# Kernel optimization log

Measured on AMD Instinct MI355X. Metric: run time of the kernel, lower is better.

## Reference

```python
import jax, jax.numpy as jnp
import numpy as np

N, F, HID, H, B = 400000, 128, 32, 4, 2000

def setup_inputs() -> dict:
    key = jax.random.key(0)
    ks = jax.random.split(key, 8)
    atom_fea = jax.random.normal(ks[0], (N, F), dtype=jnp.float32)
    segment_ids = jnp.sort(jax.random.randint(ks[1], (N,), 0, B, dtype=jnp.int32))
    s = 0.05
    return {
        "atom_fea": atom_fea,
        "segment_ids": segment_ids,
        "num_crystals": B,
        "W1": jax.random.normal(ks[2], (F, HID), dtype=jnp.float32) * s,
        "b1": jnp.zeros((HID,), dtype=jnp.float32),
        "W2": jax.random.normal(ks[3], (HID, H), dtype=jnp.float32) * s,
        "b2": jnp.zeros((H,), dtype=jnp.float32),
        "Wp": jax.random.normal(ks[4], (H * F, F), dtype=jnp.float32) * s,
        "bp": jnp.zeros((F,), dtype=jnp.float32),
    }

def reference(atom_fea, segment_ids, num_crystals, W1, b1, W2, b2, Wp, bp):
    # key MLP: (N,F) -> (N,H) attention logits (dropout is eval no-op)
    logits = jax.nn.silu(atom_fea @ W1 + b1) @ W2 + b2  # (N,H)
    # segment softmax over atoms within each crystal, per head
    seg_max = jax.ops.segment_max(logits, segment_ids, num_segments=num_crystals)
    ex = jnp.exp(logits - seg_max[segment_ids])
    denom = jax.ops.segment_sum(ex, segment_ids, num_segments=num_crystals)
    w = ex / denom[segment_ids]  # (N,H)
    # per-head softmax-weighted segment sum of atom features -> (B,H,F)
    weighted = jax.ops.segment_sum(
        w[:, :, None] * atom_fea[:, None, :], segment_ids, num_segments=num_crystals
    )
    flat = weighted.reshape(num_crystals, -1)  # (B, H*F)
    return jax.nn.silu(flat @ Wp + bp)  # (B,F)
```

## Files before the change

### kernel.cpp

```cpp
#include <hip/hip_runtime.h>
#include <math.h>

#define F 128
#define HID 32
#define NH 4
#define TILE 32
#define ROWB 512
#define PJC 4

typedef __attribute__((ext_vector_type(8))) short bf16x8;
typedef __attribute__((ext_vector_type(4))) float f32x4;

__device__ __forceinline__ float silu_f(float x) {
    return x / (1.0f + __expf(-x));
}

__device__ __forceinline__ uint f2bf(float f) {
    union { float f; uint u; } v; v.f = f;
    uint r = v.u + 0x7fffu + ((v.u >> 16) & 1u);
    return r >> 16;
}

__device__ __forceinline__ uint cvtpk_bf16(float lo, float hi) {
    uint r;
    asm("v_cvt_pk_bf16_f32 %0, %1, %2" : "=v"(r) : "v"(lo), "v"(hi));
    return r;
}

__device__ __forceinline__ void gload_lds16(const void* g, void* l) {
    __builtin_amdgcn_global_load_lds(
        (const __attribute__((address_space(1))) void*)g,
        (__attribute__((address_space(3))) void*)l, 16, 0, 0);
}

__global__ void seg_starts_kernel(const int* __restrict__ seg, int* __restrict__ starts,
                                  int N, int B) {
    int i = blockIdx.x * blockDim.x + threadIdx.x;
    if (i >= N) return;
    int id = seg[i];
    if (i == 0) {
        for (int b = 0; b <= id; ++b) starts[b] = 0;
    } else {
        int prev = seg[i - 1];
        for (int b = prev + 1; b <= id; ++b) starts[b] = i;
    }
    if (i == N - 1) {
        for (int b = id + 1; b <= B; ++b) starts[b] = N;
    }
}

__global__ __launch_bounds__(256, 4) void fused9_kernel(
    const float* __restrict__ atom_fea, const int* __restrict__ starts,
    const float* __restrict__ W1, const float* __restrict__ b1,
    const float* __restrict__ W2, const float* __restrict__ b2,
    float* __restrict__ gWacc) {
    __shared__ float sStage[2][TILE * F];
    __shared__ float sP[2 * TILE * 5];
    __shared__ float sTW[NH * 65];

    const int t = threadIdx.x;
    const int b = blockIdx.x;
    const int start = starts[b];
    const int end = starts[b + 1];
    const int wv = t >> 6;
    const int lane = t & 63;
    const int lg = lane >> 4;
    const int l15 = lane & 15;
    const int ag = wv & 1;
    const int mh = wv >> 1;
    const int ca = lane & 3;
    const int co = (lane >> 2) & 15;

    int roff[4], coff[4];
    #pragma unroll
    for (int i = 0; i < 4; ++i) {
        const int q = i * 256 + t;
        roff[i] = q >> 5;
        coff[i] = ((q & 31) ^ (roff[i] & 7)) << 4;
    }

    bf16x8 w1f[4];
    #pragma unroll
    for (int kk = 0; kk < 4; ++kk) {
        bf16x8 fr;
        #pragma unroll
        for (int j = 0; j < 8; ++j)
            fr[j] = (short)f2bf(W1[(kk * 32 + lg * 8 + j) * HID + mh * 16 + l15]);
        w1f[kk] = fr;
    }
    float b1r[4], w2r[4][4];
    #pragma unroll
    for (int r = 0; r < 4; ++r) {
        const int h = mh * 16 + lg * 4 + r;
        b1r[r] = b1[h];
        #pragma unroll
        for (int j = 0; j < 4; ++j) w2r[r][j] = W2[h * NH + j];
    }
    const float b2w = b2[wv];

    float m_run = -INFINITY;
    float s_part = 0.0f;
    float acc8[8] = {0, 0, 0, 0, 0, 0, 0, 0};

    const int nt = (end > start) ? (end - start + TILE - 1) / TILE : 0;
    const char* gbase = (const char*)atom_fea;

    if (nt > 0) {
        #pragma unroll
        for (int i = 0; i < 4; ++i) {
            int a = start + roff[i]; a = (a < end) ? a : end - 1;
            gload_lds16(gbase + (size_t)a * ROWB + coff[i],
                        (char*)sStage[0] + i * 4096 + wv * 1024);
        }
    }
    __syncthreads();

    int pb = 0;
    for (int ti = 0; ti < nt; ++ti) {
        const int base = start + ti * TILE;
        const int T = min(TILE, end - base);
        const char* bufc = (const char*)sStage[pb];
        const bool has_next = (ti + 1 < nt);

        if (has_next) {
            const int nbase = base + TILE;
            char* ldst = (char*)sStage[pb ^ 1];
            #pragma unroll
            for (int i = 0; i < 4; ++i) {
                int a = nbase + roff[i]; a = (a < end) ? a : end - 1;
                gload_lds16(gbase + (size_t)a * ROWB + coff[i],
                            ldst + i * 4096 + wv * 1024);
            }
        }

        {
            f32x4 acc;
            #pragma unroll
            for (int r = 0; r < 4; ++r) acc[r] = b1r[r];
            const int row = ag * 16 + l15;
            const char* rb = bufc + row * ROWB;
            const int rs = row & 7;
            #pragma unroll
            for (int kk = 0; kk < 4; ++kk) {
                const int c0 = kk * 8 + lg * 2;
                const float4 va = *(const float4*)(rb + ((c0 ^ rs) << 4));
                const float4 vb = *(const float4*)(rb + (((c0 + 1) ^ rs) << 4));
                union { bf16x8 v; uint u[4]; } fr;
                fr.u[0] = cvtpk_bf16(va.x, va.y);
                fr.u[1] = cvtpk_bf16(va.z, va.w);
                fr.u[2] = cvtpk_bf16(vb.x, vb.y);
                fr.u[3] = cvtpk_bf16(vb.z, vb.w);
                acc = __builtin_amdgcn_mfma_f32_16x16x32_bf16(w1f[kk], fr.v, acc, 0, 0, 0);
            }
            float p0 = 0, p1 = 0, p2 = 0, p3 = 0;
            #pragma unroll
            for (int r = 0; r < 4; ++r) {
                const float s = silu_f(acc[r]);
                p0 = fmaf(s, w2r[r][0], p0);
                p1 = fmaf(s, w2r[r][1], p1);
                p2 = fmaf(s, w2r[r][2], p2);
                p3 = fmaf(s, w2r[r][3], p3);
            }
            p0 += __shfl_xor(p0, 16); p0 += __shfl_xor(p0, 32);
            p1 += __shfl_xor(p1, 16); p1 += __shfl_xor(p1, 32);
            p2 += __shfl_xor(p2, 16); p2 += __shfl_xor(p2, 32);
            p3 += __shfl_xor(p3, 16); p3 += __shfl_xor(p3, 32);
            if (lane < 16) {
                float* d = &sP[(mh * TILE + ag * 16 + lane) * 5];
                d[0] = p0; d[1] = p1; d[2] = p2; d[3] = p3;
            }
        }
        asm volatile("s_waitcnt lgkmcnt(0)" ::: "memory");
        __builtin_amdgcn_s_barrier();

        {
            const float v = (lane < T)
                ? sP[lane * 5 + wv] + sP[(TILE + lane) * 5 + wv] + b2w
                : -INFINITY;
            if (__any(v > m_run + 8.0f)) {
                float mt = v;
                #pragma unroll
                for (int d = 1; d < 64; d <<= 1) mt = fmaxf(mt, __shfl_xor(mt, d));
                const float m_new = fmaxf(m_run, mt);
                const float r = __expf(m_run - m_new);
                s_part *= r;
                #pragma unroll
                for (int j = 0; j < 8; ++j) acc8[j] *= r;
                m_run = m_new;
            }
            const float e = (lane < T) ? __expf(v - m_run) : 0.0f;
            sTW[wv * 65 + lane] = e;
            s_part += e;
        }

        {
            #pragma unroll 4
            for (int i = 0; i < 8; ++i) {
                const int a = i * 4 + ca;
                const float w = sTW[wv * 65 + a];
                const int sw = a & 7;
                const char* ra = bufc + a * ROWB;
                const float4 v0 = *(const float4*)(ra + (((2 * co) ^ sw) << 4));
                const float4 v1 = *(const float4*)(ra + (((2 * co + 1) ^ sw) << 4));
                acc8[0] = fmaf(w, v0.x, acc8[0]);
                acc8[1] = fmaf(w, v0.y, acc8[1]);
                acc8[2] = fmaf(w, v0.z, acc8[2]);
                acc8[3] = fmaf(w, v0.w, acc8[3]);
                acc8[4] = fmaf(w, v1.x, acc8[4]);
                acc8[5] = fmaf(w, v1.y, acc8[5]);
                acc8[6] = fmaf(w, v1.z, acc8[6]);
                acc8[7] = fmaf(w, v1.w, acc8[7]);
            }
        }
        __syncthreads();
        pb ^= 1;
    }

    #pragma unroll
    for (int d = 1; d < 64; d <<= 1) s_part += __shfl_xor(s_part, d);
    const float inv = (s_part > 0.0f) ? 1.0f / s_part : 0.0f;
    #pragma unroll
    for (int j = 0; j < 8; ++j) {
        acc8[j] += __shfl_xor(acc8[j], 1);
        acc8[j] += __shfl_xor(acc8[j], 2);
    }
    if ((lane & 3) == 0) {
        float* dst = &gWacc[(size_t)b * 512 + wv * F + (lane >> 2) * 8];
        *(float4*)dst = make_float4(acc8[0] * inv, acc8[1] * inv, acc8[2] * inv, acc8[3] * inv);
        *(float4*)(dst + 4) = make_float4(acc8[4] * inv, acc8[5] * inv, acc8[6] * inv, acc8[7] * inv);
    }
}

__global__ __launch_bounds__(256) void proj_kernel(
    const float* __restrict__ gWacc, const float* __restrict__ Wp,
    const float* __restrict__ bp, float* __restrict__ out, int B) {
    __shared__ float sW[PJC * 512];
    __shared__ float sP[256 * PJC];
    const int t = threadIdx.x;
    const int c0 = blockIdx.x * PJC;
    for (int q = t; q < PJC * 512; q += 256) {
        const int cr = c0 + (q >> 9);
        sW[q] = (cr < B) ? gWacc[(size_t)cr * 512 + (q & 511)] : 0.0f;
    }
    __syncthreads();
    const int f = t & 127, half = t >> 7;
    float acc[PJC] = {};
    const float* wp = Wp + (size_t)(half * 256) * F + f;
    for (int k0 = 0; k0 < 256; k0 += 8) {
        float wpv[8];
        #pragma unroll
        for (int u = 0; u < 8; ++u) wpv[u] = wp[(size_t)(k0 + u) * F];
        #pragma unroll
        for (int u = 0; u < 8; ++u) {
            const int ks = half * 256 + k0 + u;
            #pragma unroll
            for (int g = 0; g < PJC; ++g) acc[g] = fmaf(sW[g * 512 + ks], wpv[u], acc[g]);
        }
    }
    #pragma unroll
    for (int g = 0; g < PJC; ++g) sP[t * PJC + g] = acc[g];
    __syncthreads();
    if (t < 128) {
        const float bpf = bp[t];
        #pragma unroll
        for (int g = 0; g < PJC; ++g) {
            const int cr = c0 + g;
            if (cr < B)
                out[(size_t)cr * F + t] =
                    silu_f(sP[t * PJC + g] + sP[(t + 128) * PJC + g] + bpf);
        }
    }
}

extern "C" void kernel_launch(void* const* d_in, const int* in_sizes, int n_in,
                              void* d_out, int out_size, void* d_ws, size_t ws_size,
                              hipStream_t stream) {
    const float* atom_fea = (const float*)d_in[0];
    const int* seg = (const int*)d_in[1];
    const float* W1 = (const float*)d_in[3];
    const float* b1 = (const float*)d_in[4];
    const float* W2 = (const float*)d_in[5];
    const float* b2 = (const float*)d_in[6];
    const float* Wp = (const float*)d_in[7];
    const float* bp = (const float*)d_in[8];
    float* out = (float*)d_out;

    const int N = in_sizes[0] / F;
    const int B = out_size / F;

    char* ws = (char*)d_ws;
    int* starts = (int*)ws;
    size_t off = (((size_t)(B + 1) * sizeof(int)) + 255) & ~(size_t)255;
    float* gWacc = (float*)(ws + off);

    seg_starts_kernel<<<(N + 255) / 256, 256, 0, stream>>>(seg, starts, N, B);
    fused9_kernel<<<B, 256, 0, stream>>>(atom_fea, starts, W1, b1, W2, b2, gWacc);
    proj_kernel<<<(B + PJC - 1) / PJC, 256, 0, stream>>>(gWacc, Wp, bp, out, B);
}
```

Measured before the change: 64.72 us.

## Repartition weighted-sum work: waves split atoms, lanes cover heads and feature chunks

The weighted accumulation is remapped so each wave handles a slice of 8 atoms, and the four lane groups within a wave each take one head, instead of each wave owning one head and walking all atoms. This gives every wave distinct rows of the shared-memory tile, with the same 8 rows read for all four heads, so LDS reads of atom features are shared across heads. Softmax rescale factors and the final normalisers are now passed through shared memory. The price is an extra barrier per tile and a final cross-wave reduction through LDS.

```diff
diff --git a/kernel.cpp b/kernel.cpp
--- a/kernel.cpp
+++ b/kernel.cpp
@@ -49,7 +49,7 @@
     }
 }
 
-__global__ __launch_bounds__(256, 4) void fused9_kernel(
+__global__ __launch_bounds__(256, 4) void fused10_kernel(
     const float* __restrict__ atom_fea, const int* __restrict__ starts,
     const float* __restrict__ W1, const float* __restrict__ b1,
     const float* __restrict__ W2, const float* __restrict__ b2,
@@ -57,6 +57,8 @@
     __shared__ float sStage[2][TILE * F];
     __shared__ float sP[2 * TILE * 5];
     __shared__ float sTW[NH * 65];
+    __shared__ float sR[NH];
+    __shared__ float sInv[NH];
 
     const int t = threadIdx.x;
     const int b = blockIdx.x;
@@ -68,8 +70,8 @@
     const int l15 = lane & 15;
     const int ag = wv & 1;
     const int mh = wv >> 1;
-    const int ca = lane & 3;
-    const int co = (lane >> 2) & 15;
+    const int ch = lane & 3;
+    const int co = lane >> 2;
 
     int roff[4], coff[4];
     #pragma unroll
@@ -177,27 +179,33 @@
             const float v = (lane < T)
                 ? sP[lane * 5 + wv] + sP[(TILE + lane) * 5 + wv] + b2w
                 : -INFINITY;
+            float r_t = 1.0f;
             if (__any(v > m_run + 8.0f)) {
                 float mt = v;
                 #pragma unroll
                 for (int d = 1; d < 64; d <<= 1) mt = fmaxf(mt, __shfl_xor(mt, d));
                 const float m_new = fmaxf(m_run, mt);
-                const float r = __expf(m_run - m_new);
-                s_part *= r;
-                #pragma unroll
-                for (int j = 0; j < 8; ++j) acc8[j] *= r;
+                r_t = __expf(m_run - m_new);
+                s_part *= r_t;
                 m_run = m_new;
             }
+            if (lane == 0) sR[wv] = r_t;
             const float e = (lane < T) ? __expf(v - m_run) : 0.0f;
             sTW[wv * 65 + lane] = e;
             s_part += e;
         }
+        asm volatile("s_waitcnt lgkmcnt(0)" ::: "memory");
+        __builtin_amdgcn_s_barrier();
 
         {
+            const float rr = sR[ch];
+            #pragma unroll
+            for (int j = 0; j < 8; ++j) acc8[j] *= rr;
+            const int abase = wv * 8;
             #pragma unroll 4
             for (int i = 0; i < 8; ++i) {
-                const int a = i * 4 + ca;
-                const float w = sTW[wv * 65 + a];
+                const int a = abase + i;
+                const float w = sTW[ch * 65 + a];
                 const int sw = a & 7;
                 const char* ra = bufc + a * ROWB;
                 const float4 v0 = *(const float4*)(ra + (((2 * co) ^ sw) << 4));
@@ -218,16 +226,24 @@
 
     #pragma unroll
     for (int d = 1; d < 64; d <<= 1) s_part += __shfl_xor(s_part, d);
-    const float inv = (s_part > 0.0f) ? 1.0f / s_part : 0.0f;
-    #pragma unroll
-    for (int j = 0; j < 8; ++j) {
-        acc8[j] += __shfl_xor(acc8[j], 1);
-        acc8[j] += __shfl_xor(acc8[j], 2);
-    }
-    if ((lane & 3) == 0) {
-        float* dst = &gWacc[(size_t)b * 512 + wv * F + (lane >> 2) * 8];
-        *(float4*)dst = make_float4(acc8[0] * inv, acc8[1] * inv, acc8[2] * inv, acc8[3] * inv);
-        *(float4*)(dst + 4) = make_float4(acc8[4] * inv, acc8[5] * inv, acc8[6] * inv, acc8[7] * inv);
+    if (lane == 0) sInv[wv] = (s_part > 0.0f) ? 1.0f / s_part : 0.0f;
+
+    float* red = (float*)sStage[0];
+    *(float4*)&red[(wv * 64 + lane) * 8] = make_float4(acc8[0], acc8[1], acc8[2], acc8[3]);
+    *(float4*)&red[(wv * 64 + lane) * 8 + 4] = make_float4(acc8[4], acc8[5], acc8[6], acc8[7]);
+    __syncthreads();
+    if (t < 64) {
+        const int rh = t & 3, ro = t >> 2;
+        const float inv = sInv[rh];
+        float o[8];
+        #pragma unroll
+        for (int j = 0; j < 8; ++j) {
+            o[j] = (red[(0 * 64 + t) * 8 + j] + red[(1 * 64 + t) * 8 + j] +
+                    red[(2 * 64 + t) * 8 + j] + red[(3 * 64 + t) * 8 + j]) * inv;
+        }
+        float* dst = &gWacc[(size_t)b * 512 + rh * F + ro * 8];
+        *(float4*)dst = make_float4(o[0], o[1], o[2], o[3]);
+        *(float4*)(dst + 4) = make_float4(o[4], o[5], o[6], o[7]);
     }
 }
 
@@ -294,6 +310,6 @@
     float* gWacc = (float*)(ws + off);
 
     seg_starts_kernel<<<(N + 255) / 256, 256, 0, stream>>>(seg, starts, N, B);
-    fused9_kernel<<<B, 256, 0, stream>>>(atom_fea, starts, W1, b1, W2, b2, gWacc);
+    fused10_kernel<<<B, 256, 0, stream>>>(atom_fea, starts, W1, b1, W2, b2, gWacc);
     proj_kernel<<<(B + PJC - 1) / PJC, 256, 0, stream>>>(gWacc, Wp, bp, out, B);
 }
```

Result: no change. 65.49 us (+1.2%).

## Give each wave its own row slice and merge per-wave softmax states in an epilogue

Applied to the files above, without the earlier changes.

Each of the four waves now streams and processes its own 16-row slice of a 64-row block tile into a private double buffer. It computes all 32 hidden units and all 4 head logits itself and keeps per-wave online-softmax state for every head. This removes the block-wide barriers and the cross-wave logit exchange inside the tile loop. The per-wave maxima, sums and accumulators are then combined through shared memory in a final epilogue. The cost is doubled shared memory per block (launch bounds lowered to 2 blocks), twice the MFMA work per wave, and idle waves on short segment tails.

```diff
diff --git a/kernel.cpp b/kernel.cpp
--- a/kernel.cpp
+++ b/kernel.cpp
@@ -4,7 +4,8 @@
 #define F 128
 #define HID 32
 #define NH 4
-#define TILE 32
+#define WTILE 16
+#define BTILE 64
 #define ROWB 512
 #define PJC 4
 
@@ -49,14 +50,13 @@
     }
 }
 
-__global__ __launch_bounds__(256, 4) void fused9_kernel(
+__global__ __launch_bounds__(256, 2) void fused11_kernel(
     const float* __restrict__ atom_fea, const int* __restrict__ starts,
     const float* __restrict__ W1, const float* __restrict__ b1,
     const float* __restrict__ W2, const float* __restrict__ b2,
     float* __restrict__ gWacc) {
-    __shared__ float sStage[2][TILE * F];
-    __shared__ float sP[2 * TILE * 5];
-    __shared__ float sTW[NH * 65];
+    __shared__ float sBuf[NH][2][WTILE * F];
+    __shared__ float sTW[NH][WTILE * NH];
 
     const int t = threadIdx.x;
     const int b = blockIdx.x;
@@ -66,80 +66,77 @@
     const int lane = t & 63;
     const int lg = lane >> 4;
     const int l15 = lane & 15;
-    const int ag = wv & 1;
-    const int mh = wv >> 1;
-    const int ca = lane & 3;
-    const int co = (lane >> 2) & 15;
-
-    int roff[4], coff[4];
+    const int ch = lane & 3;
+    const int co = lane >> 2;
+    const int lrh = lane >> 5;
+    const int lch = lane & 31;
+
+    bf16x8 w1f[2][4];
     #pragma unroll
-    for (int i = 0; i < 4; ++i) {
-        const int q = i * 256 + t;
-        roff[i] = q >> 5;
-        coff[i] = ((q & 31) ^ (roff[i] & 7)) << 4;
-    }
-
-    bf16x8 w1f[4];
+    for (int m0 = 0; m0 < 2; ++m0)
+        #pragma unroll
+        for (int kk = 0; kk < 4; ++kk) {
+            bf16x8 fr;
+            #pragma unroll
+            for (int j = 0; j < 8; ++j)
+                fr[j] = (short)f2bf(W1[(kk * 32 + lg * 8 + j) * HID + m0 * 16 + l15]);
+            w1f[m0][kk] = fr;
+        }
+    float b1r[8], w2r[8][4];
     #pragma unroll
-    for (int kk = 0; kk < 4; ++kk) {
-        bf16x8 fr;
-        #pragma unroll
-        for (int j = 0; j < 8; ++j)
-            fr[j] = (short)f2bf(W1[(kk * 32 + lg * 8 + j) * HID + mh * 16 + l15]);
-        w1f[kk] = fr;
-    }
-    float b1r[4], w2r[4][4];
-    #pragma unroll
-    for (int r = 0; r < 4; ++r) {
-        const int h = mh * 16 + lg * 4 + r;
-        b1r[r] = b1[h];
-        #pragma unroll
-        for (int j = 0; j < 4; ++j) w2r[r][j] = W2[h * NH + j];
-    }
-    const float b2w = b2[wv];
-
-    float m_run = -INFINITY;
-    float s_part = 0.0f;
+    for (int m0 = 0; m0 < 2; ++m0)
+        #pragma unroll
+        for (int r = 0; r < 4; ++r) {
+            const int h = m0 * 16 + lg * 4 + r;
+            b1r[m0 * 4 + r] = b1[h];
+            #pragma unroll
+            for (int j = 0; j < 4; ++j) w2r[m0 * 4 + r][j] = W2[h * NH + j];
+        }
+    const float b2r0 = b2[0], b2r1 = b2[1], b2r2 = b2[2], b2r3 = b2[3];
+
+    float m0_ = -INFINITY, m1_ = -INFINITY, m2_ = -INFINITY, m3_ = -INFINITY;
+    float s0_ = 0.0f, s1_ = 0.0f, s2_ = 0.0f, s3_ = 0.0f;
     float acc8[8] = {0, 0, 0, 0, 0, 0, 0, 0};
 
-    const int nt = (end > start) ? (end - start + TILE - 1) / TILE : 0;
-    const char* gbase = (const char*)atom_fea;
+    const int nt = (end > start) ? (end - start + BTILE - 1) / BTILE : 0;
+    const char* gb = (const char*)atom_fea;
+    char* bufA = (char*)&sBuf[wv][0][0];
+    char* bufB = (char*)&sBuf[wv][1][0];
 
     if (nt > 0) {
         #pragma unroll
-        for (int i = 0; i < 4; ++i) {
-            int a = start + roff[i]; a = (a < end) ? a : end - 1;
-            gload_lds16(gbase + (size_t)a * ROWB + coff[i],
-                        (char*)sStage[0] + i * 4096 + wv * 1024);
-        }
-    }
-    __syncthreads();
+        for (int i = 0; i < 8; ++i) {
+            const int lr = 2 * i + lrh;
+            int ga = start + wv * WTILE + lr; ga = (ga < end) ? ga : end - 1;
+            gload_lds16(gb + (size_t)ga * ROWB + ((lch ^ (lr & 7)) << 4), bufA + i * 1024);
+        }
+    }
+    asm volatile("s_waitcnt vmcnt(0)" ::: "memory");
 
     int pb = 0;
     for (int ti = 0; ti < nt; ++ti) {
-        const int base = start + ti * TILE;
-        const int T = min(TILE, end - base);
-        const char* bufc = (const char*)sStage[pb];
-        const bool has_next = (ti + 1 < nt);
-
-        if (has_next) {
-            const int nbase = base + TILE;
-            char* ldst = (char*)sStage[pb ^ 1];
-            #pragma unroll
-            for (int i = 0; i < 4; ++i) {
-                int a = nbase + roff[i]; a = (a < end) ? a : end - 1;
-                gload_lds16(gbase + (size_t)a * ROWB + coff[i],
-                            ldst + i * 4096 + wv * 1024);
-            }
-        }
-
-        {
-            f32x4 acc;
-            #pragma unroll
-            for (int r = 0; r < 4; ++r) acc[r] = b1r[r];
-            const int row = ag * 16 + l15;
-            const char* rb = bufc + row * ROWB;
-            const int rs = row & 7;
+        const int base = start + ti * BTILE;
+        const int T = min(BTILE, end - base);
+        const int Tw = min(T - wv * WTILE, WTILE);
+        char* bufc = pb ? bufB : bufA;
+
+        if (ti + 1 < nt) {
+            char* bufn = pb ? bufA : bufB;
+            const int nb = base + BTILE;
+            #pragma unroll
+            for (int i = 0; i < 8; ++i) {
+                const int lr = 2 * i + lrh;
+                int ga = nb + wv * WTILE + lr; ga = (ga < end) ? ga : end - 1;
+                gload_lds16(gb + (size_t)ga * ROWB + ((lch ^ (lr & 7)) << 4), bufn + i * 1024);
+            }
+        }
+
+        if (Tw > 0) {
+            f32x4 a0, a1;
+            #pragma unroll
+            for (int r = 0; r < 4; ++r) { a0[r] = b1r[r]; a1[r] = b1r[4 + r]; }
+            const char* rb = bufc + l15 * ROWB;
+            const int rs = l15 & 7;
             #pragma unroll
             for (int kk = 0; kk < 4; ++kk) {
                 const int c0 = kk * 8 + lg * 2;
@@ -150,84 +147,118 @@
                 fr.u[1] = cvtpk_bf16(va.z, va.w);
                 fr.u[2] = cvtpk_bf16(vb.x, vb.y);
                 fr.u[3] = cvtpk_bf16(vb.z, vb.w);
-                acc = __builtin_amdgcn_mfma_f32_16x16x32_bf16(w1f[kk], fr.v, acc, 0, 0, 0);
+                a0 = __builtin_amdgcn_mfma_f32_16x16x32_bf16(w1f[0][kk], fr.v, a0, 0, 0, 0);
+                a1 = __builtin_amdgcn_mfma_f32_16x16x32_bf16(w1f[1][kk], fr.v, a1, 0, 0, 0);
             }
             float p0 = 0, p1 = 0, p2 = 0, p3 = 0;
             #pragma unroll
             for (int r = 0; r < 4; ++r) {
-                const float s = silu_f(acc[r]);
-                p0 = fmaf(s, w2r[r][0], p0);
-                p1 = fmaf(s, w2r[r][1], p1);
-                p2 = fmaf(s, w2r[r][2], p2);
-                p3 = fmaf(s, w2r[r][3], p3);
+                const float sa = silu_f(a0[r]);
+                const float sb = silu_f(a1[r]);
+                p0 = fmaf(sa, w2r[r][0], fmaf(sb, w2r[4 + r][0], p0));
+                p1 = fmaf(sa, w2r[r][1], fmaf(sb, w2r[4 + r][1], p1));
+                p2 = fmaf(sa, w2r[r][2], fmaf(sb, w2r[4 + r][2], p2));
+                p3 = fmaf(sa, w2r[r][3], fmaf(sb, w2r[4 + r][3], p3));
             }
             p0 += __shfl_xor(p0, 16); p0 += __shfl_xor(p0, 32);
             p1 += __shfl_xor(p1, 16); p1 += __shfl_xor(p1, 32);
             p2 += __shfl_xor(p2, 16); p2 += __shfl_xor(p2, 32);
             p3 += __shfl_xor(p3, 16); p3 += __shfl_xor(p3, 32);
-            if (lane < 16) {
-                float* d = &sP[(mh * TILE + ag * 16 + lane) * 5];
-                d[0] = p0; d[1] = p1; d[2] = p2; d[3] = p3;
-            }
-        }
-        asm volatile("s_waitcnt lgkmcnt(0)" ::: "memory");
-        __builtin_amdgcn_s_barrier();
-
-        {
-            const float v = (lane < T)
-                ? sP[lane * 5 + wv] + sP[(TILE + lane) * 5 + wv] + b2w
-                : -INFINITY;
-            if (__any(v > m_run + 8.0f)) {
-                float mt = v;
+            const bool valid = (l15 < Tw);
+            const float v0 = valid ? p0 + b2r0 : -INFINITY;
+            const float v1 = valid ? p1 + b2r1 : -INFINITY;
+            const float v2 = valid ? p2 + b2r2 : -INFINITY;
+            const float v3 = valid ? p3 + b2r3 : -INFINITY;
+
+            const float dm = fmaxf(fmaxf(v0 - m0_, v1 - m1_), fmaxf(v2 - m2_, v3 - m3_));
+            if (__any(dm > 8.0f)) {
+                float t0 = v0, t1 = v1, t2 = v2, t3 = v3;
                 #pragma unroll
-                for (int d = 1; d < 64; d <<= 1) mt = fmaxf(mt, __shfl_xor(mt, d));
-                const float m_new = fmaxf(m_run, mt);
-                const float r = __expf(m_run - m_new);
-                s_part *= r;
+                for (int d = 1; d < 16; d <<= 1) {
+                    t0 = fmaxf(t0, __shfl_xor(t0, d));
+                    t1 = fmaxf(t1, __shfl_xor(t1, d));
+                    t2 = fmaxf(t2, __shfl_xor(t2, d));
+                    t3 = fmaxf(t3, __shfl_xor(t3, d));
+                }
+                const float n0 = fmaxf(m0_, t0), n1 = fmaxf(m1_, t1);
+                const float n2 = fmaxf(m2_, t2), n3 = fmaxf(m3_, t3);
+                const float r0 = __expf(m0_ - n0), r1 = __expf(m1_ - n1);
+                const float r2 = __expf(m2_ - n2), r3 = __expf(m3_ - n3);
+                s0_ *= r0; s1_ *= r1; s2_ *= r2; s3_ *= r3;
+                m0_ = n0; m1_ = n1; m2_ = n2; m3_ = n3;
+                const float rsel = (ch & 1) ? ((ch & 2) ? r3 : r1)
+                                            : ((ch & 2) ? r2 : r0);
                 #pragma unroll
-                for (int j = 0; j < 8; ++j) acc8[j] *= r;
-                m_run = m_new;
-            }
-            const float e = (lane < T) ? __expf(v - m_run) : 0.0f;
-            sTW[wv * 65 + lane] = e;
-            s_part += e;
-        }
-
-        {
-            #pragma unroll 4
-            for (int i = 0; i < 8; ++i) {
-                const int a = i * 4 + ca;
-                const float w = sTW[wv * 65 + a];
+                for (int j = 0; j < 8; ++j) acc8[j] *= rsel;
+            }
+            const float e0 = valid ? __expf(v0 - m0_) : 0.0f;
+            const float e1 = valid ? __expf(v1 - m1_) : 0.0f;
+            const float e2 = valid ? __expf(v2 - m2_) : 0.0f;
+            const float e3 = valid ? __expf(v3 - m3_) : 0.0f;
+            s0_ += e0; s1_ += e1; s2_ += e2; s3_ += e3;
+            if (lane < 16) *(float4*)&sTW[wv][lane * NH] = make_float4(e0, e1, e2, e3);
+
+            #pragma unroll 8
+            for (int a = 0; a < WTILE; ++a) {
+                const float w = sTW[wv][a * NH + ch];
                 const int sw = a & 7;
                 const char* ra = bufc + a * ROWB;
-                const float4 v0 = *(const float4*)(ra + (((2 * co) ^ sw) << 4));
-                const float4 v1 = *(const float4*)(ra + (((2 * co + 1) ^ sw) << 4));
-                acc8[0] = fmaf(w, v0.x, acc8[0]);
-                acc8[1] = fmaf(w, v0.y, acc8[1]);
-                acc8[2] = fmaf(w, v0.z, acc8[2]);
-                acc8[3] = fmaf(w, v0.w, acc8[3]);
-                acc8[4] = fmaf(w, v1.x, acc8[4]);
-                acc8[5] = fmaf(w, v1.y, acc8[5]);
-                acc8[6] = fmaf(w, v1.z, acc8[6]);
-                acc8[7] = fmaf(w, v1.w, acc8[7]);
-            }
-        }
-        __syncthreads();
+                const float4 q0 = *(const float4*)(ra + (((2 * co) ^ sw) << 4));
+                const float4 q1 = *(const float4*)(ra + (((2 * co + 1) ^ sw) << 4));
+                acc8[0] = fmaf(w, q0.x, acc8[0]);
+                acc8[1] = fmaf(w, q0.y, acc8[1]);
+                acc8[2] = fmaf(w, q0.z, acc8[2]);
+                acc8[3] = fmaf(w, q0.w, acc8[3]);
+                acc8[4] = fmaf(w, q1.x, acc8[4]);
+                acc8[5] = fmaf(w, q1.y, acc8[5]);
+                acc8[6] = fmaf(w, q1.z, acc8[6]);
+                acc8[7] = fmaf(w, q1.w, acc8[7]);
+            }
+        }
+        asm volatile("s_waitcnt vmcnt(0)" ::: "memory");
         pb ^= 1;
     }
 
     #pragma unroll
-    for (int d = 1; d < 64; d <<= 1) s_part += __shfl_xor(s_part, d);
-    const float inv = (s_part > 0.0f) ? 1.0f / s_part : 0.0f;
-    #pragma unroll
-    for (int j = 0; j < 8; ++j) {
-        acc8[j] += __shfl_xor(acc8[j], 1);
-        acc8[j] += __shfl_xor(acc8[j], 2);
-    }
-    if ((lane & 3) == 0) {
-        float* dst = &gWacc[(size_t)b * 512 + wv * F + (lane >> 2) * 8];
-        *(float4*)dst = make_float4(acc8[0] * inv, acc8[1] * inv, acc8[2] * inv, acc8[3] * inv);
-        *(float4*)(dst + 4) = make_float4(acc8[4] * inv, acc8[5] * inv, acc8[6] * inv, acc8[7] * inv);
+    for (int d = 1; d < 64; d <<= 1) {
+        s0_ += __shfl_xor(s0_, d); s1_ += __shfl_xor(s1_, d);
+        s2_ += __shfl_xor(s2_, d); s3_ += __shfl_xor(s3_, d);
+    }
+    float* epi = &sBuf[wv][0][0];
+    *(float4*)&epi[lane * 8] = make_float4(acc8[0], acc8[1], acc8[2], acc8[3]);
+    *(float4*)&epi[lane * 8 + 4] = make_float4(acc8[4], acc8[5], acc8[6], acc8[7]);
+    if (lane == 0) {
+        epi[512] = m0_; epi[513] = m1_; epi[514] = m2_; epi[515] = m3_;
+        epi[516] = s0_ * 0.25f; epi[517] = s1_ * 0.25f;
+        epi[518] = s2_ * 0.25f; epi[519] = s3_ * 0.25f;
+    }
+    __syncthreads();
+    if (t < 64) {
+        const int ch2 = t & 3, co2 = t >> 2;
+        float mw[NH], fw[NH];
+        float mg = -INFINITY;
+        #pragma unroll
+        for (int w = 0; w < NH; ++w) {
+            mw[w] = sBuf[w][0][512 + ch2];
+            mg = fmaxf(mg, mw[w]);
+        }
+        float sg = 0.0f;
+        #pragma unroll
+        for (int w = 0; w < NH; ++w) {
+            fw[w] = (mw[w] == -INFINITY) ? 0.0f : __expf(mw[w] - mg);
+            sg += sBuf[w][0][516 + ch2] * fw[w];
+        }
+        const float inv = (sg > 0.0f) ? 1.0f / sg : 0.0f;
+        float o[8] = {0, 0, 0, 0, 0, 0, 0, 0};
+        #pragma unroll
+        for (int w = 0; w < NH; ++w) {
+            const float* ap = &sBuf[w][0][t * 8];
+            #pragma unroll
+            for (int j = 0; j < 8; ++j) o[j] = fmaf(ap[j], fw[w], o[j]);
+        }
+        float* dst = &gWacc[(size_t)b * 512 + ch2 * F + co2 * 8];
+        *(float4*)dst = make_float4(o[0] * inv, o[1] * inv, o[2] * inv, o[3] * inv);
+        *(float4*)(dst + 4) = make_float4(o[4] * inv, o[5] * inv, o[6] * inv, o[7] * inv);
     }
 }
 
@@ -294,6 +325,6 @@
     float* gWacc = (float*)(ws + off);
 
     seg_starts_kernel<<<(N + 255) / 256, 256, 0, stream>>>(seg, starts, N, B);
-    fused9_kernel<<<B, 256, 0, stream>>>(atom_fea, starts, W1, b1, W2, b2, gWacc);
+    fused11_kernel<<<B, 256, 0, stream>>>(atom_fea, starts, W1, b1, W2, b2, gWacc);
     proj_kernel<<<(B + PJC - 1) / PJC, 256, 0, stream>>>(gWacc, Wp, bp, out, B);
 }
```

Result: slower. 70.38 us (+8.7%).

## Split each segment across two blocks with online-softmax partial merge in projection

Applied to the files above, without the earlier changes.

Each crystal segment is now processed by two blocks, each covering half of the atoms. Each block writes unnormalized weighted sums plus its running max and exp-sum per head. The projection kernel merges the two partials flash-attention style before the matmul. This doubles the grid from 2000 to 4000 blocks for better CU occupancy and load balance. The cost is extra partial-buffer traffic and merge work in the projection kernel.

```diff
diff --git a/kernel.cpp b/kernel.cpp
--- a/kernel.cpp
+++ b/kernel.cpp
@@ -7,6 +7,7 @@
 #define TILE 32
 #define ROWB 512
 #define PJC 4
+#define PSLOT 520
 
 typedef __attribute__((ext_vector_type(8))) short bf16x8;
 typedef __attribute__((ext_vector_type(4))) float f32x4;
@@ -49,19 +50,26 @@
     }
 }
 
-__global__ __launch_bounds__(256, 4) void fused9_kernel(
+__global__ __launch_bounds__(256, 4) void fused13_kernel(
     const float* __restrict__ atom_fea, const int* __restrict__ starts,
     const float* __restrict__ W1, const float* __restrict__ b1,
     const float* __restrict__ W2, const float* __restrict__ b2,
-    float* __restrict__ gWacc) {
+    float* __restrict__ gPart) {
     __shared__ float sStage[2][TILE * F];
     __shared__ float sP[2 * TILE * 5];
     __shared__ float sTW[NH * 65];
 
     const int t = threadIdx.x;
-    const int b = blockIdx.x;
-    const int start = starts[b];
-    const int end = starts[b + 1];
+    const int bid = blockIdx.x;
+    const int b = bid >> 1;
+    const int half = bid & 1;
+    const int s0 = starts[b];
+    const int e0 = starts[b + 1];
+    const int len = e0 - s0;
+    const int hl = (len + 1) >> 1;
+    const int start = half ? (s0 + hl) : s0;
+    const int end = half ? e0 : (s0 + hl);
+
     const int wv = t >> 6;
     const int lane = t & 63;
     const int lg = lane >> 4;
@@ -218,31 +226,56 @@
 
     #pragma unroll
     for (int d = 1; d < 64; d <<= 1) s_part += __shfl_xor(s_part, d);
-    const float inv = (s_part > 0.0f) ? 1.0f / s_part : 0.0f;
     #pragma unroll
     for (int j = 0; j < 8; ++j) {
         acc8[j] += __shfl_xor(acc8[j], 1);
         acc8[j] += __shfl_xor(acc8[j], 2);
     }
+    float* slot = &gPart[(size_t)bid * PSLOT];
     if ((lane & 3) == 0) {
-        float* dst = &gWacc[(size_t)b * 512 + wv * F + (lane >> 2) * 8];
-        *(float4*)dst = make_float4(acc8[0] * inv, acc8[1] * inv, acc8[2] * inv, acc8[3] * inv);
-        *(float4*)(dst + 4) = make_float4(acc8[4] * inv, acc8[5] * inv, acc8[6] * inv, acc8[7] * inv);
-    }
-}
-
-__global__ __launch_bounds__(256) void proj_kernel(
-    const float* __restrict__ gWacc, const float* __restrict__ Wp,
+        float* dst = slot + wv * F + (lane >> 2) * 8;
+        *(float4*)dst = make_float4(acc8[0], acc8[1], acc8[2], acc8[3]);
+        *(float4*)(dst + 4) = make_float4(acc8[4], acc8[5], acc8[6], acc8[7]);
+    }
+    if (lane == 0) {
+        slot[512 + wv] = m_run;
+        slot[516 + wv] = s_part;
+    }
+}
+
+__global__ __launch_bounds__(256) void proj2_kernel(
+    const float* __restrict__ gPart, const float* __restrict__ Wp,
     const float* __restrict__ bp, float* __restrict__ out, int B) {
+    __shared__ float sRaw[PJC][2][PSLOT];
     __shared__ float sW[PJC * 512];
     __shared__ float sP[256 * PJC];
     const int t = threadIdx.x;
     const int c0 = blockIdx.x * PJC;
+
+    for (int q = t; q < PJC * 2 * PSLOT; q += 256) {
+        const int g = q / (2 * PSLOT);
+        const int rem = q - g * 2 * PSLOT;
+        const int hf = rem / PSLOT;
+        const int k = rem - hf * PSLOT;
+        const int cr = c0 + g;
+        sRaw[g][hf][k] = (cr < B) ? gPart[(size_t)(cr * 2 + hf) * PSLOT + k] : 0.0f;
+    }
+    __syncthreads();
+
     for (int q = t; q < PJC * 512; q += 256) {
-        const int cr = c0 + (q >> 9);
-        sW[q] = (cr < B) ? gWacc[(size_t)cr * 512 + (q & 511)] : 0.0f;
+        const int g = q >> 9;
+        const int k = q & 511;
+        const int h = k >> 7;
+        const float m0 = sRaw[g][0][512 + h], m1 = sRaw[g][1][512 + h];
+        const float mg = fmaxf(m0, m1);
+        const float f0 = (m0 == -INFINITY) ? 0.0f : __expf(m0 - mg);
+        const float f1 = (m1 == -INFINITY) ? 0.0f : __expf(m1 - mg);
+        const float sg = sRaw[g][0][516 + h] * f0 + sRaw[g][1][516 + h] * f1;
+        const float inv = (sg > 0.0f) ? 1.0f / sg : 0.0f;
+        sW[q] = (sRaw[g][0][k] * f0 + sRaw[g][1][k] * f1) * inv;
     }
     __syncthreads();
+
     const int f = t & 127, half = t >> 7;
     float acc[PJC] = {};
     const float* wp = Wp + (size_t)(half * 256) * F + f;
@@ -291,9 +324,9 @@
     char* ws = (char*)d_ws;
     int* starts = (int*)ws;
     size_t off = (((size_t)(B + 1) * sizeof(int)) + 255) & ~(size_t)255;
-    float* gWacc = (float*)(ws + off);
+    float* gPart = (float*)(ws + off);
 
     seg_starts_kernel<<<(N + 255) / 256, 256, 0, stream>>>(seg, starts, N, B);
-    fused9_kernel<<<B, 256, 0, stream>>>(atom_fea, starts, W1, b1, W2, b2, gWacc);
-    proj_kernel<<<(B + PJC - 1) / PJC, 256, 0, stream>>>(gWacc, Wp, bp, out, B);
-}
+    fused13_kernel<<<2 * B, 256, 0, stream>>>(atom_fea, starts, W1, b1, W2, b2, gPart);
+    proj2_kernel<<<(B + PJC - 1) / PJC, 256, 0, stream>>>(gPart, Wp, bp, out, B);
+}
```

Measured after the change: 71.94 us. 11.2% more time.
